# Performance work log

Measured on AMD Instinct MI355X. Metric: run time of the kernel, lower is better.

## Reference

```python
import jax, jax.numpy as jnp
import numpy as np

B, L, D = 16, 4096, 512


def setup_inputs() -> dict:
    key = jax.random.key(0)
    ks = jax.random.split(key, 8)
    s = 1.0 / np.sqrt(D)
    x = jax.random.normal(ks[0], (B, L, D), dtype=jnp.float32)
    Wk = jax.random.normal(ks[1], (D, D), dtype=jnp.float32) * s
    Wq = jax.random.normal(ks[2], (D, D), dtype=jnp.float32) * s
    Wv = jax.random.normal(ks[3], (D, D), dtype=jnp.float32) * s
    bk = jnp.zeros((D,), jnp.float32)
    bq = jnp.zeros((D,), jnp.float32)
    bv = jnp.zeros((D,), jnp.float32)
    lens = jax.random.randint(ks[4], (B,), 1, L + 1, dtype=jnp.int32)
    return {"x": x, "Wk": Wk, "bk": bk, "Wq": Wq, "bq": bq,
            "Wv": Wv, "bv": bv, "lens": lens}


def reference(x, Wk, bk, Wq, bq, Wv, bv, lens):
    # Dropout is identity in eval mode.
    x_k = jnp.tanh(jnp.einsum('bld,ed->ble', x, Wk) + bk)  # [B,L,D]
    x_q = jnp.tanh(jnp.einsum('bld,ed->ble', x, Wq) + bq)
    x_v = jnp.tanh(jnp.einsum('bld,ed->ble', x, Wv) + bv)
    # sum_j (x_k_i . x_q_j) == x_k_i . sum_j x_q_j  (algebraic collapse of the L x L bmm)
    q_sum = x_q.sum(axis=1)                                # [B,D]
    w = jnp.einsum('bld,bd->bl', x_k, q_sum) / (D ** 0.5)  # [B,L]
    pad = jnp.arange(L)[None, :] >= lens[:, None]          # True at padding
    w = jnp.where(pad, -jnp.inf, w)
    w = jax.nn.softmax(w, axis=1)                          # [B,L]
    # (x_v * w[...,None]).sum(-1) == x_v.sum(-1) * w
    return x_v.sum(axis=-1) * w                            # [B,L]
```

## Files before the change

kernel.cpp:

```cpp
#include <hip/hip_runtime.h>
#include <hip/hip_bf16.h>

typedef __attribute__((ext_vector_type(4)))  int   i32x4;
typedef __attribute__((ext_vector_type(16))) int   i32x16;
typedef __attribute__((ext_vector_type(16))) float f32x16;
typedef __attribute__((ext_vector_type(8)))  short short8;

#define SC1 (1.0f/4096.0f)
#define SC2 (1.0f/524288.0f)

static __device__ __forceinline__ float ftanh(float x) {
  float e = __builtin_amdgcn_exp2f(x * 2.885390081777927f);
  return 1.0f - 2.0f * __builtin_amdgcn_rcpf(e + 1.0f);
}
static __device__ __forceinline__ unsigned short bf16_rn(float f) {
  unsigned u = __float_as_uint(f);
  u += 0x7FFFu + ((u >> 16) & 1u);
  return (unsigned short)(u >> 16);
}
static __device__ __forceinline__ void quant2(float x, float sc, float inv, float losc,
                                              int& hi, int& lo) {
  float t  = __builtin_fmaf(x, sc, 12582912.0f);
  hi = __float_as_int(t) - 0x4B400000;
  float hf = t - 12582912.0f;
  float r  = __builtin_fmaf(hf, -inv, x);
  float t2 = __builtin_fmaf(r, losc, 12582912.0f);
  lo = __float_as_int(t2) - 0x4B400000;
}
static __device__ __forceinline__ void gll16(const void* g, void* l) {
  __builtin_amdgcn_global_load_lds((const __attribute__((address_space(1))) unsigned int*)g,
                                   (__attribute__((address_space(3))) unsigned int*)l, 16, 0, 0);
}
#define MFMA_I8(ACC, A, B) \
  asm("v_mfma_i32_32x32x32_i8 %0, %1, %2, %0" : "+v"(ACC) : "v"(A), "v"(B))

__global__ void prep_w(const float* __restrict__ Wq, const float* __restrict__ Wk,
                       const float* __restrict__ Wv,
                       char* __restrict__ B1, char* __restrict__ B2) {
  int gid = blockIdx.x * 256 + threadIdx.x;
  if (gid < 65536) {
    int chunk = gid >> 12, g = gid & 4095;
    char* dst = B1 + chunk * 65536 + g * 16;
    if (g < 2048) {
      int sel = g >> 10;
      int gg = g & 1023, nt = gg >> 6, lane = gg & 63;
      const float* src = Wq + (size_t)(nt * 32 + (lane & 31)) * 512 + chunk * 32 + (lane >> 5) * 16;
      union { char b[16]; i32x4 v; } ob;
#pragma unroll
      for (int j = 0; j < 16; ++j) {
        int h, l; quant2(src[j], 256.f, 1.f / 256.f, 32768.f, h, l);
        ob.b[j] = (char)(sel ? l : h);
      }
      *(i32x4*)dst = ob.v;
    } else {
      int gg = g - 2048, nt = gg >> 7, ks = (gg >> 6) & 1, lane = gg & 63;
      const float* src = Wv + (size_t)(nt * 32 + (lane & 31)) * 512 + chunk * 32 + ks * 16 + (lane >> 5) * 8;
      union { unsigned short s[8]; i32x4 v; } ob;
#pragma unroll
      for (int j = 0; j < 8; ++j) ob.s[j] = bf16_rn(src[j]);
      *(i32x4*)dst = ob.v;
    }
  } else {
    int gid2 = gid - 65536;
    int chunk = gid2 >> 11, g = gid2 & 2047;
    char* dst = B2 + chunk * 32768 + g * 16;
    int sel = g >> 10, gg = g & 1023, nt = gg >> 6, lane = gg & 63;
    const float* src = Wk + (size_t)(nt * 32 + (lane & 31)) * 512 + chunk * 32 + (lane >> 5) * 16;
    union { char b[16]; i32x4 v; } ob;
#pragma unroll
    for (int j = 0; j < 16; ++j) {
      int h, l; quant2(src[j], 256.f, 1.f / 256.f, 32768.f, h, l);
      ob.b[j] = (char)(sel ? l : h);
    }
    *(i32x4*)dst = ob.v;
  }
}

static __device__ __forceinline__ void stageAi8(char* Ab, int tid, float4 xv) {
  const int row = tid >> 3, d0 = (tid & 7) * 4;
  const int mt = row >> 5, l31 = row & 31;
  int h0, l0, h1, l1, h2, l2, h3, l3;
  quant2(xv.x, 16.f, 0.0625f, 2048.f, h0, l0);
  quant2(xv.y, 16.f, 0.0625f, 2048.f, h1, l1);
  quant2(xv.z, 16.f, 0.0625f, 2048.f, h2, l2);
  quant2(xv.w, 16.f, 0.0625f, 2048.f, h3, l3);
  unsigned wh = (h0 & 255) | ((h1 & 255) << 8) | ((h2 & 255) << 16) | ((unsigned)(h3 & 255) << 24);
  unsigned wl = (l0 & 255) | ((l1 & 255) << 8) | ((l2 & 255) << 16) | ((unsigned)(l3 & 255) << 24);
  const int lane8 = (d0 >> 4) * 32 + l31, j = d0 & 15;
  *(unsigned*)(Ab + (mt * 64 + lane8) * 16 + j) = wh;
  *(unsigned*)(Ab + 2048 + (mt * 64 + lane8) * 16 + j) = wl;
}

static __device__ __forceinline__ void stageAv(char* Ab, int tid, float4 xv) {
  const int row = tid >> 3, d0 = (tid & 7) * 4;
  const int mt = row >> 5, l31 = row & 31;
  unsigned long long b0 = bf16_rn(xv.x), b1 = bf16_rn(xv.y), b2 = bf16_rn(xv.z), b3 = bf16_rn(xv.w);
  unsigned long long vv = b0 | (b1 << 16) | (b2 << 32) | (b3 << 48);
  const int ks = d0 >> 4, rem = d0 & 15, hs8 = rem >> 3, j8 = rem & 7;
  *(unsigned long long*)(Ab + ((mt * 2 + ks) * 64 + hs8 * 32 + l31) * 16 + j8 * 2) = vv;
}

__global__ __launch_bounds__(512, 2) void pass_q(
    const float* __restrict__ x, const char* __restrict__ B1,
    const float* __restrict__ bq, float* __restrict__ qpart) {
  extern __shared__ char smem[];
  char* Bb0 = smem;            char* Bb1 = smem + 32768;
  char* Ab0 = smem + 65536;    char* Ab1 = smem + 69632;

  const int tid = threadIdx.x, lane = tid & 63, w = tid >> 6;
  const int l31 = lane & 31;
  const float* xrow = x + ((size_t)blockIdx.x * 64 + (tid >> 3)) * 512 + (tid & 7) * 4;

  i32x16 q1[2][2] = {}; i32x16 q2[2][2] = {};

  float4 xcur = *(const float4*)(xrow);
  stageAi8(Ab0, tid, xcur);
  {
    const char* src = B1 + tid * 16;
    char* dst = Bb0 + tid * 16;
#pragma unroll
    for (int i = 0; i < 4; ++i) gll16(src + i * 8192, dst + i * 8192);
  }
  xcur = *(const float4*)(xrow + 32);

#pragma unroll 1
  for (int c = 0; c < 16; ++c) {
    const int p = c & 1;
    char* Bc = p ? Bb1 : Bb0;  char* Bn = p ? Bb0 : Bb1;
    char* Ac = p ? Ab1 : Ab0;  char* An = p ? Ab0 : Ab1;
    __syncthreads();
    if (c < 15) {
      const char* src = B1 + (size_t)(c + 1) * 65536 + tid * 16;
      char* dst = Bn + tid * 16;
#pragma unroll
      for (int i = 0; i < 4; ++i) gll16(src + i * 8192, dst + i * 8192);
    }
    float4 xnext = xcur;
    if (c < 14) xnext = *(const float4*)(xrow + (c + 2) * 32);
    if (c < 15) stageAi8(An, tid, xcur);

    const int lo16 = lane * 16;
    i32x4 aqh0 = *(const i32x4*)(Ac + lo16);
    i32x4 aqh1 = *(const i32x4*)(Ac + 1024 + lo16);
    i32x4 aql0 = *(const i32x4*)(Ac + 2048 + lo16);
    i32x4 aql1 = *(const i32x4*)(Ac + 3072 + lo16);
    __builtin_amdgcn_s_setprio(1);
#pragma unroll
    for (int nn = 0; nn < 2; ++nn) {
      const int nt = w * 2 + nn;
      i32x4 bh = *(const i32x4*)(Bc + nt * 1024 + lo16);
      i32x4 bl = *(const i32x4*)(Bc + 16384 + nt * 1024 + lo16);
      MFMA_I8(q1[0][nn], aqh0, bh);
      MFMA_I8(q2[0][nn], aqh0, bl);
      MFMA_I8(q2[0][nn], aql0, bh);
      MFMA_I8(q1[1][nn], aqh1, bh);
      MFMA_I8(q2[1][nn], aqh1, bl);
      MFMA_I8(q2[1][nn], aql1, bh);
    }
    __builtin_amdgcn_s_setprio(0);
    xcur = xnext;
  }

#pragma unroll
  for (int nn = 0; nn < 2; ++nn) {
    const int col = (w * 2 + nn) * 32 + l31;
    const float bc = bq[col];
    float cs = 0.f;
#pragma unroll
    for (int mt = 0; mt < 2; ++mt)
#pragma unroll
      for (int r = 0; r < 16; ++r)
        cs += ftanh(__builtin_fmaf((float)q1[mt][nn][r], SC1,
                    __builtin_fmaf((float)q2[mt][nn][r], SC2, bc)));
    cs += __shfl_xor(cs, 32);
    if (lane < 32) qpart[(size_t)blockIdx.x * 512 + col] = cs;
  }
}

__global__ __launch_bounds__(512, 2) void pass_v(
    const float* __restrict__ x, const char* __restrict__ B1,
    const float* __restrict__ bv, float* __restrict__ svout) {
  extern __shared__ char smem[];
  char* Bb0 = smem;            char* Bb1 = smem + 32768;
  char* Ab0 = smem + 65536;    char* Ab1 = smem + 69632;
  float* redv = (float*)(smem + 73728);

  const int tid = threadIdx.x, lane = tid & 63, w = tid >> 6;
  const int l31 = lane & 31, hs = lane >> 5;
  const float* xrow = x + ((size_t)blockIdx.x * 64 + (tid >> 3)) * 512 + (tid & 7) * 4;

  f32x16 accv[2][2] = {};

  float4 xcur = *(const float4*)(xrow);
  stageAv(Ab0, tid, xcur);
  {
    const char* src = B1 + 32768 + tid * 16;
    char* dst = Bb0 + tid * 16;
#pragma unroll
    for (int i = 0; i < 4; ++i) gll16(src + i * 8192, dst + i * 8192);
  }
  xcur = *(const float4*)(xrow + 32);

#pragma unroll 1
  for (int c = 0; c < 16; ++c) {
    const int p = c & 1;
    char* Bc = p ? Bb1 : Bb0;  char* Bn = p ? Bb0 : Bb1;
    char* Ac = p ? Ab1 : Ab0;  char* An = p ? Ab0 : Ab1;
    __syncthreads();
    if (c < 15) {
      const char* src = B1 + (size_t)(c + 1) * 65536 + 32768 + tid * 16;
      char* dst = Bn + tid * 16;
#pragma unroll
      for (int i = 0; i < 4; ++i) gll16(src + i * 8192, dst + i * 8192);
    }
    float4 xnext = xcur;
    if (c < 14) xnext = *(const float4*)(xrow + (c + 2) * 32);
    if (c < 15) stageAv(An, tid, xcur);

    const int lo16 = lane * 16;
    __builtin_amdgcn_s_setprio(1);
#pragma unroll
    for (int ks = 0; ks < 2; ++ks) {
      short8 av0 = *(const short8*)(Ac + (0 * 2 + ks) * 1024 + lo16);
      short8 av1 = *(const short8*)(Ac + (1 * 2 + ks) * 1024 + lo16);
#pragma unroll
      for (int nn = 0; nn < 2; ++nn) {
        const int nt = w * 2 + nn;
        short8 bvf = *(const short8*)(Bc + (nt * 2 + ks) * 1024 + lo16);
        accv[0][nn] = __builtin_amdgcn_mfma_f32_32x32x16_bf16(av0, bvf, accv[0][nn], 0, 0, 0);
        accv[1][nn] = __builtin_amdgcn_mfma_f32_32x32x16_bf16(av1, bvf, accv[1][nn], 0, 0, 0);
      }
    }
    __builtin_amdgcn_s_setprio(0);
    xcur = xnext;
  }

  const float bv0 = bv[(w * 2 + 0) * 32 + l31];
  const float bv1 = bv[(w * 2 + 1) * 32 + l31];
  __syncthreads();
#pragma unroll
  for (int mt = 0; mt < 2; ++mt)
#pragma unroll
    for (int r = 0; r < 16; ++r) {
      float s = ftanh(accv[mt][0][r] + bv0) + ftanh(accv[mt][1][r] + bv1);
#pragma unroll
      for (int off = 1; off <= 16; off <<= 1) s += __shfl_xor(s, off);
      if (l31 == 0) redv[w * 64 + mt * 32 + (r & 3) + 8 * (r >> 2) + 4 * hs] = s;
    }
  __syncthreads();
  if (tid < 64) {
    float s = 0.f;
#pragma unroll
    for (int j = 0; j < 8; ++j) s += redv[j * 64 + tid];
    svout[(size_t)blockIdx.x * 64 + tid] = s;
  }
}

__global__ __launch_bounds__(512, 2) void pass_k(
    const float* __restrict__ x, const char* __restrict__ B2,
    const float* __restrict__ bk, const float* __restrict__ q_sum,
    float* __restrict__ scores) {
  extern __shared__ char smem[];
  char* Bb0 = smem;           char* Bb1 = smem + 32768;
  char* Ab0 = smem + 65536;   char* Ab1 = smem + 69632;
  float* redk = (float*)(smem + 73728);

  const int tid = threadIdx.x, lane = tid & 63, w = tid >> 6;
  const int l31 = lane & 31, hs = lane >> 5;
  const float* xrow = x + ((size_t)blockIdx.x * 64 + (tid >> 3)) * 512 + (tid & 7) * 4;

  i32x16 k1[2][2] = {}; i32x16 k2[2][2] = {};

  float4 xcur = *(const float4*)(xrow);
  stageAi8(Ab0, tid, xcur);
  {
    const char* src = B2 + tid * 16;
    char* dst = Bb0 + tid * 16;
#pragma unroll
    for (int i = 0; i < 4; ++i) gll16(src + i * 8192, dst + i * 8192);
  }
  xcur = *(const float4*)(xrow + 32);

#pragma unroll 1
  for (int c = 0; c < 16; ++c) {
    const int p = c & 1;
    char* Bc = p ? Bb1 : Bb0;  char* Bn = p ? Bb0 : Bb1;
    char* Ac = p ? Ab1 : Ab0;  char* An = p ? Ab0 : Ab1;
    __syncthreads();
    if (c < 15) {
      const char* src = B2 + (size_t)(c + 1) * 32768 + tid * 16;
      char* dst = Bn + tid * 16;
#pragma unroll
      for (int i = 0; i < 4; ++i) gll16(src + i * 8192, dst + i * 8192);
    }
    float4 xnext = xcur;
    if (c < 14) xnext = *(const float4*)(xrow + (c + 2) * 32);
    if (c < 15) stageAi8(An, tid, xcur);

    const int lo16 = lane * 16;
    i32x4 ah0 = *(const i32x4*)(Ac + lo16);
    i32x4 ah1 = *(const i32x4*)(Ac + 1024 + lo16);
    i32x4 al0 = *(const i32x4*)(Ac + 2048 + lo16);
    i32x4 al1 = *(const i32x4*)(Ac + 3072 + lo16);
    __builtin_amdgcn_s_setprio(1);
#pragma unroll
    for (int nn = 0; nn < 2; ++nn) {
      const int nt = w * 2 + nn;
      i32x4 bh = *(const i32x4*)(Bc + nt * 1024 + lo16);
      i32x4 bl = *(const i32x4*)(Bc + 16384 + nt * 1024 + lo16);
      MFMA_I8(k1[0][nn], ah0, bh);
      MFMA_I8(k2[0][nn], ah0, bl);
      MFMA_I8(k2[0][nn], al0, bh);
      MFMA_I8(k1[1][nn], ah1, bh);
      MFMA_I8(k2[1][nn], ah1, bl);
      MFMA_I8(k2[1][nn], al1, bh);
    }
    __builtin_amdgcn_s_setprio(0);
    xcur = xnext;
  }

  const int b = blockIdx.x >> 6;
  const int c0 = (w * 2 + 0) * 32 + l31, c1 = (w * 2 + 1) * 32 + l31;
  const float qs0 = q_sum[b * 512 + c0], qs1 = q_sum[b * 512 + c1];
  const float bk0 = bk[c0], bk1 = bk[c1];
  __syncthreads();
#pragma unroll
  for (int mt = 0; mt < 2; ++mt)
#pragma unroll
    for (int r = 0; r < 16; ++r) {
      float p0 = __builtin_fmaf((float)k1[mt][0][r], SC1,
                 __builtin_fmaf((float)k2[mt][0][r], SC2, bk0));
      float p1 = __builtin_fmaf((float)k1[mt][1][r], SC1,
                 __builtin_fmaf((float)k2[mt][1][r], SC2, bk1));
      float s = ftanh(p0) * qs0 + ftanh(p1) * qs1;
#pragma unroll
      for (int off = 1; off <= 16; off <<= 1) s += __shfl_xor(s, off);
      if (l31 == 0) redk[w * 64 + mt * 32 + (r & 3) + 8 * (r >> 2) + 4 * hs] = s;
    }
  __syncthreads();
  if (tid < 64) {
    float s = 0.f;
#pragma unroll
    for (int j = 0; j < 8; ++j) s += redk[j * 64 + tid];
    scores[(size_t)blockIdx.x * 64 + tid] = s;
  }
}

__global__ void reduce_q(const float* __restrict__ qpart, float* __restrict__ q_sum) {
  int b = blockIdx.x, e = threadIdx.x;
  const float* p = qpart + (size_t)b * 64 * 512 + e;
  float s = 0.f;
#pragma unroll 4
  for (int j = 0; j < 64; ++j) s += p[j * 512];
  q_sum[b * 512 + e] = s;
}

__global__ void softmax_out(const float* __restrict__ scores,
                            const float* __restrict__ sv,
                            const int* __restrict__ lens,
                            float* __restrict__ out) {
  const int b = blockIdx.x, tid = threadIdx.x;
  const int lane = tid & 63, wid = tid >> 6;
  const int len = lens[b];
  const float scale = 0.04419417382415922f;
  __shared__ float sb[4], sb2[4];

  float sreg[16];
  const float* sc = scores + (size_t)b * 4096;
#pragma unroll
  for (int j = 0; j < 16; ++j) sreg[j] = sc[tid + j * 256] * scale;

  float m = -1e30f;
#pragma unroll
  for (int j = 0; j < 16; ++j)
    if (tid + j * 256 < len) m = fmaxf(m, sreg[j]);
#pragma unroll
  for (int off = 32; off >= 1; off >>= 1) m = fmaxf(m, __shfl_xor(m, off));
  if (lane == 0) sb[wid] = m;
  __syncthreads();
  m = fmaxf(fmaxf(sb[0], sb[1]), fmaxf(sb[2], sb[3]));

  float s = 0.f;
#pragma unroll
  for (int j = 0; j < 16; ++j)
    if (tid + j * 256 < len) s += expf(sreg[j] - m);
#pragma unroll
  for (int off = 32; off >= 1; off >>= 1) s += __shfl_xor(s, off);
  if (lane == 0) sb2[wid] = s;
  __syncthreads();
  const float inv = 1.f / (sb2[0] + sb2[1] + sb2[2] + sb2[3]);

  const float* svb = sv + (size_t)b * 4096;
  float* ob = out + (size_t)b * 4096;
#pragma unroll
  for (int j = 0; j < 16; ++j) {
    int l = tid + j * 256;
    ob[l] = (l < len) ? svb[l] * expf(sreg[j] - m) * inv : 0.0f;
  }
}

extern "C" void kernel_launch(void* const* d_in, const int* in_sizes, int n_in,
                              void* d_out, int out_size, void* d_ws, size_t ws_size,
                              hipStream_t stream) {
  const float* x  = (const float*)d_in[0];
  const float* Wk = (const float*)d_in[1];
  const float* bk = (const float*)d_in[2];
  const float* Wq = (const float*)d_in[3];
  const float* bq = (const float*)d_in[4];
  const float* Wv = (const float*)d_in[5];
  const float* bv = (const float*)d_in[6];
  const int* lens = (const int*)d_in[7];
  float* out = (float*)d_out;

  char* ws = (char*)d_ws;
  char*  B1     = ws;
  char*  B2     = ws + 1048576;
  float* qpart  = (float*)(ws + 1572864);
  float* q_sum  = (float*)(ws + 3670016);
  float* svbuf  = (float*)(ws + 3702784);
  float* scores = (float*)(ws + 3964928);

  prep_w<<<384, 256, 0, stream>>>(Wq, Wk, Wv, B1, B2);
  pass_q<<<1024, 512, 73728, stream>>>(x, B1, bq, qpart);
  pass_v<<<1024, 512, 75776, stream>>>(x, B1, bv, svbuf);
  reduce_q<<<16, 512, 0, stream>>>(qpart, q_sum);
  pass_k<<<1024, 512, 75776, stream>>>(x, B2, bk, q_sum, scores);
  softmax_out<<<16, 256, 0, stream>>>(scores, svbuf, lens, out);
}
```

Baseline: 246.3 us.

## Split the projection passes into four column-group blocks with smaller LDS footprint

Each of pass_q, pass_v and pass_k now launches 4096 blocks of 256 threads, and each block computes a 128-column slice of the output instead of all 512 columns. This shrinks LDS per block and lets more blocks fit per CU, aiming for better latency hiding. The V and K passes now write per-column-group partial sums, which softmax_out adds together. The cost is that every x tile is read and quantized four times per pass, which relies on cache reuse to avoid extra HBM traffic. The s_setprio hints are also removed.

Result: slower. 300.6 us (+22.0%).

```diff
diff --git a/kernel.cpp b/kernel.cpp
--- a/kernel.cpp
+++ b/kernel.cpp
@@ -76,8 +76,7 @@
   }
 }
 
-static __device__ __forceinline__ void stageAi8(char* Ab, int tid, float4 xv) {
-  const int row = tid >> 3, d0 = (tid & 7) * 4;
+static __device__ __forceinline__ void stA8(char* Ab, int row, int d0, float4 xv) {
   const int mt = row >> 5, l31 = row & 31;
   int h0, l0, h1, l1, h2, l2, h3, l3;
   quant2(xv.x, 16.f, 0.0625f, 2048.f, h0, l0);
@@ -90,9 +89,7 @@
   *(unsigned*)(Ab + (mt * 64 + lane8) * 16 + j) = wh;
   *(unsigned*)(Ab + 2048 + (mt * 64 + lane8) * 16 + j) = wl;
 }
-
-static __device__ __forceinline__ void stageAv(char* Ab, int tid, float4 xv) {
-  const int row = tid >> 3, d0 = (tid & 7) * 4;
+static __device__ __forceinline__ void stAv(char* Ab, int row, int d0, float4 xv) {
   const int mt = row >> 5, l31 = row & 31;
   unsigned long long b0 = bf16_rn(xv.x), b1 = bf16_rn(xv.y), b2 = bf16_rn(xv.z), b3 = bf16_rn(xv.w);
   unsigned long long vv = b0 | (b1 << 16) | (b2 << 32) | (b3 << 48);
@@ -100,28 +97,31 @@
   *(unsigned long long*)(Ab + ((mt * 2 + ks) * 64 + hs8 * 32 + l31) * 16 + j8 * 2) = vv;
 }
 
-__global__ __launch_bounds__(512, 2) void pass_q(
+__global__ __launch_bounds__(256, 3) void pass_q(
     const float* __restrict__ x, const char* __restrict__ B1,
     const float* __restrict__ bq, float* __restrict__ qpart) {
   extern __shared__ char smem[];
-  char* Bb0 = smem;            char* Bb1 = smem + 32768;
-  char* Ab0 = smem + 65536;    char* Ab1 = smem + 69632;
+  char* Bb0 = smem;           char* Bb1 = smem + 8192;
+  char* Ab0 = smem + 16384;   char* Ab1 = smem + 20480;
 
   const int tid = threadIdx.x, lane = tid & 63, w = tid >> 6;
   const int l31 = lane & 31;
-  const float* xrow = x + ((size_t)blockIdx.x * 64 + (tid >> 3)) * 512 + (tid & 7) * 4;
-
-  i32x16 q1[2][2] = {}; i32x16 q2[2][2] = {};
-
-  float4 xcur = *(const float4*)(xrow);
-  stageAi8(Ab0, tid, xcur);
+  const int tile = blockIdx.x & 1023, cg = blockIdx.x >> 10;
+  const int row = tid >> 2, d0 = (tid & 3) * 8;
+  const float* gxr = x + ((size_t)tile * 64 + row) * 512 + d0;
+
+  i32x16 q1[2] = {}, q2[2] = {};
+
+  float4 xa = *(const float4*)(gxr);
+  float4 xb = *(const float4*)(gxr + 4);
+  stA8(Ab0, row, d0, xa); stA8(Ab0, row, d0 + 4, xb);
   {
-    const char* src = B1 + tid * 16;
-    char* dst = Bb0 + tid * 16;
-#pragma unroll
-    for (int i = 0; i < 4; ++i) gll16(src + i * 8192, dst + i * 8192);
-  }
-  xcur = *(const float4*)(xrow + 32);
+    const char* src = B1 + cg * 4096 + tid * 16;
+    gll16(src, Bb0 + tid * 16);
+    gll16(src + 16384, Bb0 + 4096 + tid * 16);
+  }
+  xa = *(const float4*)(gxr + 32);
+  xb = *(const float4*)(gxr + 36);
 
 #pragma unroll 1
   for (int c = 0; c < 16; ++c) {
@@ -130,76 +130,72 @@
     char* Ac = p ? Ab1 : Ab0;  char* An = p ? Ab0 : Ab1;
     __syncthreads();
     if (c < 15) {
-      const char* src = B1 + (size_t)(c + 1) * 65536 + tid * 16;
-      char* dst = Bn + tid * 16;
-#pragma unroll
-      for (int i = 0; i < 4; ++i) gll16(src + i * 8192, dst + i * 8192);
-    }
-    float4 xnext = xcur;
-    if (c < 14) xnext = *(const float4*)(xrow + (c + 2) * 32);
-    if (c < 15) stageAi8(An, tid, xcur);
+      const char* src = B1 + (size_t)(c + 1) * 65536 + cg * 4096 + tid * 16;
+      gll16(src, Bn + tid * 16);
+      gll16(src + 16384, Bn + 4096 + tid * 16);
+    }
+    float4 xna = xa, xnb = xb;
+    if (c < 14) {
+      xna = *(const float4*)(gxr + (c + 2) * 32);
+      xnb = *(const float4*)(gxr + (c + 2) * 32 + 4);
+    }
+    if (c < 15) { stA8(An, row, d0, xa); stA8(An, row, d0 + 4, xb); }
 
     const int lo16 = lane * 16;
-    i32x4 aqh0 = *(const i32x4*)(Ac + lo16);
-    i32x4 aqh1 = *(const i32x4*)(Ac + 1024 + lo16);
-    i32x4 aql0 = *(const i32x4*)(Ac + 2048 + lo16);
-    i32x4 aql1 = *(const i32x4*)(Ac + 3072 + lo16);
-    __builtin_amdgcn_s_setprio(1);
-#pragma unroll
-    for (int nn = 0; nn < 2; ++nn) {
-      const int nt = w * 2 + nn;
-      i32x4 bh = *(const i32x4*)(Bc + nt * 1024 + lo16);
-      i32x4 bl = *(const i32x4*)(Bc + 16384 + nt * 1024 + lo16);
-      MFMA_I8(q1[0][nn], aqh0, bh);
-      MFMA_I8(q2[0][nn], aqh0, bl);
-      MFMA_I8(q2[0][nn], aql0, bh);
-      MFMA_I8(q1[1][nn], aqh1, bh);
-      MFMA_I8(q2[1][nn], aqh1, bl);
-      MFMA_I8(q2[1][nn], aql1, bh);
-    }
-    __builtin_amdgcn_s_setprio(0);
-    xcur = xnext;
-  }
-
-#pragma unroll
-  for (int nn = 0; nn < 2; ++nn) {
-    const int col = (w * 2 + nn) * 32 + l31;
-    const float bc = bq[col];
-    float cs = 0.f;
-#pragma unroll
-    for (int mt = 0; mt < 2; ++mt)
-#pragma unroll
-      for (int r = 0; r < 16; ++r)
-        cs += ftanh(__builtin_fmaf((float)q1[mt][nn][r], SC1,
-                    __builtin_fmaf((float)q2[mt][nn][r], SC2, bc)));
-    cs += __shfl_xor(cs, 32);
-    if (lane < 32) qpart[(size_t)blockIdx.x * 512 + col] = cs;
-  }
-}
-
-__global__ __launch_bounds__(512, 2) void pass_v(
+    i32x4 ah0 = *(const i32x4*)(Ac + lo16);
+    i32x4 ah1 = *(const i32x4*)(Ac + 1024 + lo16);
+    i32x4 al0 = *(const i32x4*)(Ac + 2048 + lo16);
+    i32x4 al1 = *(const i32x4*)(Ac + 3072 + lo16);
+    i32x4 bh = *(const i32x4*)(Bc + w * 1024 + lo16);
+    i32x4 bl = *(const i32x4*)(Bc + 4096 + w * 1024 + lo16);
+    MFMA_I8(q1[0], ah0, bh);
+    MFMA_I8(q2[0], ah0, bl);
+    MFMA_I8(q2[0], al0, bh);
+    MFMA_I8(q1[1], ah1, bh);
+    MFMA_I8(q2[1], ah1, bl);
+    MFMA_I8(q2[1], al1, bh);
+    xa = xna; xb = xnb;
+  }
+
+  const int col = cg * 128 + w * 32 + l31;
+  const float bc = bq[col];
+  float cs = 0.f;
+#pragma unroll
+  for (int mt = 0; mt < 2; ++mt)
+#pragma unroll
+    for (int r = 0; r < 16; ++r)
+      cs += ftanh(__builtin_fmaf((float)q1[mt][r], SC1,
+                  __builtin_fmaf((float)q2[mt][r], SC2, bc)));
+  cs += __shfl_xor(cs, 32);
+  if (lane < 32) qpart[(size_t)tile * 512 + col] = cs;
+}
+
+__global__ __launch_bounds__(256, 4) void pass_v(
     const float* __restrict__ x, const char* __restrict__ B1,
-    const float* __restrict__ bv, float* __restrict__ svout) {
+    const float* __restrict__ bv, float* __restrict__ vpart) {
   extern __shared__ char smem[];
-  char* Bb0 = smem;            char* Bb1 = smem + 32768;
-  char* Ab0 = smem + 65536;    char* Ab1 = smem + 69632;
-  float* redv = (float*)(smem + 73728);
+  char* Bb0 = smem;           char* Bb1 = smem + 8192;
+  char* Ab0 = smem + 16384;   char* Ab1 = smem + 20480;
+  float* redv = (float*)(smem + 24576);
 
   const int tid = threadIdx.x, lane = tid & 63, w = tid >> 6;
   const int l31 = lane & 31, hs = lane >> 5;
-  const float* xrow = x + ((size_t)blockIdx.x * 64 + (tid >> 3)) * 512 + (tid & 7) * 4;
-
-  f32x16 accv[2][2] = {};
-
-  float4 xcur = *(const float4*)(xrow);
-  stageAv(Ab0, tid, xcur);
+  const int tile = blockIdx.x & 1023, cg = blockIdx.x >> 10;
+  const int row = tid >> 2, d0 = (tid & 3) * 8;
+  const float* gxr = x + ((size_t)tile * 64 + row) * 512 + d0;
+
+  f32x16 accv[2] = {};
+
+  float4 xa = *(const float4*)(gxr);
+  float4 xb = *(const float4*)(gxr + 4);
+  stAv(Ab0, row, d0, xa); stAv(Ab0, row, d0 + 4, xb);
   {
-    const char* src = B1 + 32768 + tid * 16;
-    char* dst = Bb0 + tid * 16;
-#pragma unroll
-    for (int i = 0; i < 4; ++i) gll16(src + i * 8192, dst + i * 8192);
-  }
-  xcur = *(const float4*)(xrow + 32);
+    const char* src = B1 + 32768 + cg * 8192 + tid * 16;
+    gll16(src, Bb0 + tid * 16);
+    gll16(src + 4096, Bb0 + 4096 + tid * 16);
+  }
+  xa = *(const float4*)(gxr + 32);
+  xb = *(const float4*)(gxr + 36);
 
 #pragma unroll 1
   for (int c = 0; c < 16; ++c) {
@@ -208,78 +204,74 @@
     char* Ac = p ? Ab1 : Ab0;  char* An = p ? Ab0 : Ab1;
     __syncthreads();
     if (c < 15) {
-      const char* src = B1 + (size_t)(c + 1) * 65536 + 32768 + tid * 16;
-      char* dst = Bn + tid * 16;
-#pragma unroll
-      for (int i = 0; i < 4; ++i) gll16(src + i * 8192, dst + i * 8192);
-    }
-    float4 xnext = xcur;
-    if (c < 14) xnext = *(const float4*)(xrow + (c + 2) * 32);
-    if (c < 15) stageAv(An, tid, xcur);
+      const char* src = B1 + (size_t)(c + 1) * 65536 + 32768 + cg * 8192 + tid * 16;
+      gll16(src, Bn + tid * 16);
+      gll16(src + 4096, Bn + 4096 + tid * 16);
+    }
+    float4 xna = xa, xnb = xb;
+    if (c < 14) {
+      xna = *(const float4*)(gxr + (c + 2) * 32);
+      xnb = *(const float4*)(gxr + (c + 2) * 32 + 4);
+    }
+    if (c < 15) { stAv(An, row, d0, xa); stAv(An, row, d0 + 4, xb); }
 
     const int lo16 = lane * 16;
-    __builtin_amdgcn_s_setprio(1);
 #pragma unroll
     for (int ks = 0; ks < 2; ++ks) {
       short8 av0 = *(const short8*)(Ac + (0 * 2 + ks) * 1024 + lo16);
       short8 av1 = *(const short8*)(Ac + (1 * 2 + ks) * 1024 + lo16);
-#pragma unroll
-      for (int nn = 0; nn < 2; ++nn) {
-        const int nt = w * 2 + nn;
-        short8 bvf = *(const short8*)(Bc + (nt * 2 + ks) * 1024 + lo16);
-        accv[0][nn] = __builtin_amdgcn_mfma_f32_32x32x16_bf16(av0, bvf, accv[0][nn], 0, 0, 0);
-        accv[1][nn] = __builtin_amdgcn_mfma_f32_32x32x16_bf16(av1, bvf, accv[1][nn], 0, 0, 0);
-      }
-    }
-    __builtin_amdgcn_s_setprio(0);
-    xcur = xnext;
-  }
-
-  const float bv0 = bv[(w * 2 + 0) * 32 + l31];
-  const float bv1 = bv[(w * 2 + 1) * 32 + l31];
+      short8 bvf = *(const short8*)(Bc + (w * 2 + ks) * 1024 + lo16);
+      accv[0] = __builtin_amdgcn_mfma_f32_32x32x16_bf16(av0, bvf, accv[0], 0, 0, 0);
+      accv[1] = __builtin_amdgcn_mfma_f32_32x32x16_bf16(av1, bvf, accv[1], 0, 0, 0);
+    }
+    xa = xna; xb = xnb;
+  }
+
+  const float bvc = bv[cg * 128 + w * 32 + l31];
   __syncthreads();
 #pragma unroll
   for (int mt = 0; mt < 2; ++mt)
 #pragma unroll
     for (int r = 0; r < 16; ++r) {
-      float s = ftanh(accv[mt][0][r] + bv0) + ftanh(accv[mt][1][r] + bv1);
+      float s = ftanh(accv[mt][r] + bvc);
 #pragma unroll
       for (int off = 1; off <= 16; off <<= 1) s += __shfl_xor(s, off);
       if (l31 == 0) redv[w * 64 + mt * 32 + (r & 3) + 8 * (r >> 2) + 4 * hs] = s;
     }
   __syncthreads();
   if (tid < 64) {
-    float s = 0.f;
-#pragma unroll
-    for (int j = 0; j < 8; ++j) s += redv[j * 64 + tid];
-    svout[(size_t)blockIdx.x * 64 + tid] = s;
-  }
-}
-
-__global__ __launch_bounds__(512, 2) void pass_k(
+    float s = redv[tid] + redv[64 + tid] + redv[128 + tid] + redv[192 + tid];
+    vpart[(size_t)cg * 65536 + (size_t)tile * 64 + tid] = s;
+  }
+}
+
+__global__ __launch_bounds__(256, 3) void pass_k(
     const float* __restrict__ x, const char* __restrict__ B2,
     const float* __restrict__ bk, const float* __restrict__ q_sum,
-    float* __restrict__ scores) {
+    float* __restrict__ spart) {
   extern __shared__ char smem[];
-  char* Bb0 = smem;           char* Bb1 = smem + 32768;
-  char* Ab0 = smem + 65536;   char* Ab1 = smem + 69632;
-  float* redk = (float*)(smem + 73728);
+  char* Bb0 = smem;           char* Bb1 = smem + 8192;
+  char* Ab0 = smem + 16384;   char* Ab1 = smem + 20480;
+  float* redk = (float*)(smem + 24576);
 
   const int tid = threadIdx.x, lane = tid & 63, w = tid >> 6;
   const int l31 = lane & 31, hs = lane >> 5;
-  const float* xrow = x + ((size_t)blockIdx.x * 64 + (tid >> 3)) * 512 + (tid & 7) * 4;
-
-  i32x16 k1[2][2] = {}; i32x16 k2[2][2] = {};
-
-  float4 xcur = *(const float4*)(xrow);
-  stageAi8(Ab0, tid, xcur);
+  const int tile = blockIdx.x & 1023, cg = blockIdx.x >> 10;
+  const int row = tid >> 2, d0 = (tid & 3) * 8;
+  const float* gxr = x + ((size_t)tile * 64 + row) * 512 + d0;
+
+  i32x16 k1[2] = {}, k2[2] = {};
+
+  float4 xa = *(const float4*)(gxr);
+  float4 xb = *(const float4*)(gxr + 4);
+  stA8(Ab0, row, d0, xa); stA8(Ab0, row, d0 + 4, xb);
   {
-    const char* src = B2 + tid * 16;
-    char* dst = Bb0 + tid * 16;
-#pragma unroll
-    for (int i = 0; i < 4; ++i) gll16(src + i * 8192, dst + i * 8192);
-  }
-  xcur = *(const float4*)(xrow + 32);
+    const char* src = B2 + cg * 4096 + tid * 16;
+    gll16(src, Bb0 + tid * 16);
+    gll16(src + 16384, Bb0 + 4096 + tid * 16);
+  }
+  xa = *(const float4*)(gxr + 32);
+  xb = *(const float4*)(gxr + 36);
 
 #pragma unroll 1
   for (int c = 0; c < 16; ++c) {
@@ -288,61 +280,53 @@
     char* Ac = p ? Ab1 : Ab0;  char* An = p ? Ab0 : Ab1;
     __syncthreads();
     if (c < 15) {
-      const char* src = B2 + (size_t)(c + 1) * 32768 + tid * 16;
-      char* dst = Bn + tid * 16;
-#pragma unroll
-      for (int i = 0; i < 4; ++i) gll16(src + i * 8192, dst + i * 8192);
-    }
-    float4 xnext = xcur;
-    if (c < 14) xnext = *(const float4*)(xrow + (c + 2) * 32);
-    if (c < 15) stageAi8(An, tid, xcur);
+      const char* src = B2 + (size_t)(c + 1) * 32768 + cg * 4096 + tid * 16;
+      gll16(src, Bn + tid * 16);
+      gll16(src + 16384, Bn + 4096 + tid * 16);
+    }
+    float4 xna = xa, xnb = xb;
+    if (c < 14) {
+      xna = *(const float4*)(gxr + (c + 2) * 32);
+      xnb = *(const float4*)(gxr + (c + 2) * 32 + 4);
+    }
+    if (c < 15) { stA8(An, row, d0, xa); stA8(An, row, d0 + 4, xb); }
 
     const int lo16 = lane * 16;
     i32x4 ah0 = *(const i32x4*)(Ac + lo16);
     i32x4 ah1 = *(const i32x4*)(Ac + 1024 + lo16);
     i32x4 al0 = *(const i32x4*)(Ac + 2048 + lo16);
     i32x4 al1 = *(const i32x4*)(Ac + 3072 + lo16);
-    __builtin_amdgcn_s_setprio(1);
-#pragma unroll
-    for (int nn = 0; nn < 2; ++nn) {
-      const int nt = w * 2 + nn;
-      i32x4 bh = *(const i32x4*)(Bc + nt * 1024 + lo16);
-      i32x4 bl = *(const i32x4*)(Bc + 16384 + nt * 1024 + lo16);
-      MFMA_I8(k1[0][nn], ah0, bh);
-      MFMA_I8(k2[0][nn], ah0, bl);
-      MFMA_I8(k2[0][nn], al0, bh);
-      MFMA_I8(k1[1][nn], ah1, bh);
-      MFMA_I8(k2[1][nn], ah1, bl);
-      MFMA_I8(k2[1][nn], al1, bh);
-    }
-    __builtin_amdgcn_s_setprio(0);
-    xcur = xnext;
-  }
-
-  const int b = blockIdx.x >> 6;
-  const int c0 = (w * 2 + 0) * 32 + l31, c1 = (w * 2 + 1) * 32 + l31;
-  const float qs0 = q_sum[b * 512 + c0], qs1 = q_sum[b * 512 + c1];
-  const float bk0 = bk[c0], bk1 = bk[c1];
+    i32x4 bh = *(const i32x4*)(Bc + w * 1024 + lo16);
+    i32x4 bl = *(const i32x4*)(Bc + 4096 + w * 1024 + lo16);
+    MFMA_I8(k1[0], ah0, bh);
+    MFMA_I8(k2[0], ah0, bl);
+    MFMA_I8(k2[0], al0, bh);
+    MFMA_I8(k1[1], ah1, bh);
+    MFMA_I8(k2[1], ah1, bl);
+    MFMA_I8(k2[1], al1, bh);
+    xa = xna; xb = xnb;
+  }
+
+  const int b = tile >> 6;
+  const int col = cg * 128 + w * 32 + l31;
+  const float qs = q_sum[b * 512 + col];
+  const float bkc = bk[col];
   __syncthreads();
 #pragma unroll
   for (int mt = 0; mt < 2; ++mt)
 #pragma unroll
     for (int r = 0; r < 16; ++r) {
-      float p0 = __builtin_fmaf((float)k1[mt][0][r], SC1,
-                 __builtin_fmaf((float)k2[mt][0][r], SC2, bk0));
-      float p1 = __builtin_fmaf((float)k1[mt][1][r], SC1,
-                 __builtin_fmaf((float)k2[mt][1][r], SC2, bk1));
-      float s = ftanh(p0) * qs0 + ftanh(p1) * qs1;
+      float pre = __builtin_fmaf((float)k1[mt][r], SC1,
+                  __builtin_fmaf((float)k2[mt][r], SC2, bkc));
+      float s = ftanh(pre) * qs;
 #pragma unroll
       for (int off = 1; off <= 16; off <<= 1) s += __shfl_xor(s, off);
       if (l31 == 0) redk[w * 64 + mt * 32 + (r & 3) + 8 * (r >> 2) + 4 * hs] = s;
     }
   __syncthreads();
   if (tid < 64) {
-    float s = 0.f;
-#pragma unroll
-    for (int j = 0; j < 8; ++j) s += redk[j * 64 + tid];
-    scores[(size_t)blockIdx.x * 64 + tid] = s;
+    float s = redk[tid] + redk[64 + tid] + redk[128 + tid] + redk[192 + tid];
+    spart[(size_t)cg * 65536 + (size_t)tile * 64 + tid] = s;
   }
 }
 
@@ -355,8 +339,8 @@
   q_sum[b * 512 + e] = s;
 }
 
-__global__ void softmax_out(const float* __restrict__ scores,
-                            const float* __restrict__ sv,
+__global__ void softmax_out(const float* __restrict__ spart,
+                            const float* __restrict__ vpart,
                             const int* __restrict__ lens,
                             float* __restrict__ out) {
   const int b = blockIdx.x, tid = threadIdx.x;
@@ -365,10 +349,13 @@
   const float scale = 0.04419417382415922f;
   __shared__ float sb[4], sb2[4];
 
-  float sreg[16];
-  const float* sc = scores + (size_t)b * 4096;
-#pragma unroll
-  for (int j = 0; j < 16; ++j) sreg[j] = sc[tid + j * 256] * scale;
+  float sreg[16], svreg[16];
+#pragma unroll
+  for (int j = 0; j < 16; ++j) {
+    size_t l = (size_t)b * 4096 + tid + j * 256;
+    sreg[j] = (spart[l] + spart[65536 + l] + spart[131072 + l] + spart[196608 + l]) * scale;
+    svreg[j] = vpart[l] + vpart[65536 + l] + vpart[131072 + l] + vpart[196608 + l];
+  }
 
   float m = -1e30f;
 #pragma unroll
@@ -390,12 +377,11 @@
   __syncthreads();
   const float inv = 1.f / (sb2[0] + sb2[1] + sb2[2] + sb2[3]);
 
-  const float* svb = sv + (size_t)b * 4096;
   float* ob = out + (size_t)b * 4096;
 #pragma unroll
   for (int j = 0; j < 16; ++j) {
     int l = tid + j * 256;
-    ob[l] = (l < len) ? svb[l] * expf(sreg[j] - m) * inv : 0.0f;
+    ob[l] = (l < len) ? svreg[j] * expf(sreg[j] - m) * inv : 0.0f;
   }
 }
 
@@ -417,13 +403,13 @@
   char*  B2     = ws + 1048576;
   float* qpart  = (float*)(ws + 1572864);
   float* q_sum  = (float*)(ws + 3670016);
-  float* svbuf  = (float*)(ws + 3702784);
-  float* scores = (float*)(ws + 3964928);
+  float* vpart  = (float*)(ws + 3702784);
+  float* spart  = (float*)(ws + 4751360);
 
   prep_w<<<384, 256, 0, stream>>>(Wq, Wk, Wv, B1, B2);
-  pass_q<<<1024, 512, 73728, stream>>>(x, B1, bq, qpart);
-  pass_v<<<1024, 512, 75776, stream>>>(x, B1, bv, svbuf);
+  pass_q<<<4096, 256, 24576, stream>>>(x, B1, bq, qpart);
+  pass_v<<<4096, 256, 25600, stream>>>(x, B1, bv, vpart);
   reduce_q<<<16, 512, 0, stream>>>(qpart, q_sum);
-  pass_k<<<1024, 512, 75776, stream>>>(x, B2, bk, q_sum, scores);
-  softmax_out<<<16, 256, 0, stream>>>(scores, svbuf, lens, out);
-}
+  pass_k<<<4096, 256, 25600, stream>>>(x, B2, bk, q_sum, spart);
+  softmax_out<<<16, 256, 0, stream>>>(spart, vpart, lens, out);
+}
```

## Halve row tile to 32 per block and double grid size

Applied to the files above, without the earlier changes.

Each of the three projection passes now handles 32 rows of x per block instead of 64, giving 2048 blocks, and only half the threads stage A. The full 512-column weight slab is still streamed into LDS per block, so total weight traffic through L2/LDS doubles relative to x rows. Launch bounds ask for 4 blocks per CU and setprio hints are removed, and reduce_q sums 128 partials. This trades weight reuse per block for more blocks and fewer accumulator registers per thread, but LDS use per block (~69KB) still limits residency.

Result: slower. 263.5 us (+7.0%).

```diff
diff --git a/kernel.cpp b/kernel.cpp
--- a/kernel.cpp
+++ b/kernel.cpp
@@ -76,9 +76,7 @@
   }
 }
 
-static __device__ __forceinline__ void stageAi8(char* Ab, int tid, float4 xv) {
-  const int row = tid >> 3, d0 = (tid & 7) * 4;
-  const int mt = row >> 5, l31 = row & 31;
+static __device__ __forceinline__ void stA8_32(char* Ab, int row, int d0, float4 xv) {
   int h0, l0, h1, l1, h2, l2, h3, l3;
   quant2(xv.x, 16.f, 0.0625f, 2048.f, h0, l0);
   quant2(xv.y, 16.f, 0.0625f, 2048.f, h1, l1);
@@ -86,42 +84,41 @@
   quant2(xv.w, 16.f, 0.0625f, 2048.f, h3, l3);
   unsigned wh = (h0 & 255) | ((h1 & 255) << 8) | ((h2 & 255) << 16) | ((unsigned)(h3 & 255) << 24);
   unsigned wl = (l0 & 255) | ((l1 & 255) << 8) | ((l2 & 255) << 16) | ((unsigned)(l3 & 255) << 24);
-  const int lane8 = (d0 >> 4) * 32 + l31, j = d0 & 15;
-  *(unsigned*)(Ab + (mt * 64 + lane8) * 16 + j) = wh;
-  *(unsigned*)(Ab + 2048 + (mt * 64 + lane8) * 16 + j) = wl;
-}
-
-static __device__ __forceinline__ void stageAv(char* Ab, int tid, float4 xv) {
-  const int row = tid >> 3, d0 = (tid & 7) * 4;
-  const int mt = row >> 5, l31 = row & 31;
+  const int lane8 = (d0 >> 4) * 32 + row, j = d0 & 15;
+  *(unsigned*)(Ab + lane8 * 16 + j) = wh;
+  *(unsigned*)(Ab + 1024 + lane8 * 16 + j) = wl;
+}
+static __device__ __forceinline__ void stAv_32(char* Ab, int row, int d0, float4 xv) {
   unsigned long long b0 = bf16_rn(xv.x), b1 = bf16_rn(xv.y), b2 = bf16_rn(xv.z), b3 = bf16_rn(xv.w);
   unsigned long long vv = b0 | (b1 << 16) | (b2 << 32) | (b3 << 48);
   const int ks = d0 >> 4, rem = d0 & 15, hs8 = rem >> 3, j8 = rem & 7;
-  *(unsigned long long*)(Ab + ((mt * 2 + ks) * 64 + hs8 * 32 + l31) * 16 + j8 * 2) = vv;
-}
-
-__global__ __launch_bounds__(512, 2) void pass_q(
+  *(unsigned long long*)(Ab + (ks * 64 + hs8 * 32 + row) * 16 + j8 * 2) = vv;
+}
+
+__global__ __launch_bounds__(512, 4) void pass_q(
     const float* __restrict__ x, const char* __restrict__ B1,
     const float* __restrict__ bq, float* __restrict__ qpart) {
   extern __shared__ char smem[];
-  char* Bb0 = smem;            char* Bb1 = smem + 32768;
-  char* Ab0 = smem + 65536;    char* Ab1 = smem + 69632;
+  char* Bb0 = smem;          char* Bb1 = smem + 32768;
+  char* Ab0 = smem + 65536;  char* Ab1 = smem + 67584;
 
   const int tid = threadIdx.x, lane = tid & 63, w = tid >> 6;
   const int l31 = lane & 31;
-  const float* xrow = x + ((size_t)blockIdx.x * 64 + (tid >> 3)) * 512 + (tid & 7) * 4;
-
-  i32x16 q1[2][2] = {}; i32x16 q2[2][2] = {};
-
-  float4 xcur = *(const float4*)(xrow);
-  stageAi8(Ab0, tid, xcur);
+  const int tile = blockIdx.x;
+  const int row = tid >> 3, d0 = (tid & 7) * 4;
+  const float* gxr = x + ((size_t)tile * 32 + row) * 512 + d0;
+
+  i32x16 q1[2] = {}, q2[2] = {};
+  float4 xcur = {};
+
+  if (tid < 256) { xcur = *(const float4*)(gxr); stA8_32(Ab0, row, d0, xcur); }
   {
     const char* src = B1 + tid * 16;
     char* dst = Bb0 + tid * 16;
 #pragma unroll
     for (int i = 0; i < 4; ++i) gll16(src + i * 8192, dst + i * 8192);
   }
-  xcur = *(const float4*)(xrow + 32);
+  if (tid < 256) xcur = *(const float4*)(gxr + 32);
 
 #pragma unroll 1
   for (int c = 0; c < 16; ++c) {
@@ -136,28 +133,23 @@
       for (int i = 0; i < 4; ++i) gll16(src + i * 8192, dst + i * 8192);
     }
     float4 xnext = xcur;
-    if (c < 14) xnext = *(const float4*)(xrow + (c + 2) * 32);
-    if (c < 15) stageAi8(An, tid, xcur);
+    if (tid < 256) {
+      if (c < 14) xnext = *(const float4*)(gxr + (c + 2) * 32);
+      if (c < 15) stA8_32(An, row, d0, xcur);
+    }
 
     const int lo16 = lane * 16;
-    i32x4 aqh0 = *(const i32x4*)(Ac + lo16);
-    i32x4 aqh1 = *(const i32x4*)(Ac + 1024 + lo16);
-    i32x4 aql0 = *(const i32x4*)(Ac + 2048 + lo16);
-    i32x4 aql1 = *(const i32x4*)(Ac + 3072 + lo16);
-    __builtin_amdgcn_s_setprio(1);
+    i32x4 ah = *(const i32x4*)(Ac + lo16);
+    i32x4 al = *(const i32x4*)(Ac + 1024 + lo16);
 #pragma unroll
     for (int nn = 0; nn < 2; ++nn) {
       const int nt = w * 2 + nn;
       i32x4 bh = *(const i32x4*)(Bc + nt * 1024 + lo16);
       i32x4 bl = *(const i32x4*)(Bc + 16384 + nt * 1024 + lo16);
-      MFMA_I8(q1[0][nn], aqh0, bh);
-      MFMA_I8(q2[0][nn], aqh0, bl);
-      MFMA_I8(q2[0][nn], aql0, bh);
-      MFMA_I8(q1[1][nn], aqh1, bh);
-      MFMA_I8(q2[1][nn], aqh1, bl);
-      MFMA_I8(q2[1][nn], aql1, bh);
-    }
-    __builtin_amdgcn_s_setprio(0);
+      MFMA_I8(q1[nn], ah, bh);
+      MFMA_I8(q2[nn], ah, bl);
+      MFMA_I8(q2[nn], al, bh);
+    }
     xcur = xnext;
   }
 
@@ -167,39 +159,39 @@
     const float bc = bq[col];
     float cs = 0.f;
 #pragma unroll
-    for (int mt = 0; mt < 2; ++mt)
-#pragma unroll
-      for (int r = 0; r < 16; ++r)
-        cs += ftanh(__builtin_fmaf((float)q1[mt][nn][r], SC1,
-                    __builtin_fmaf((float)q2[mt][nn][r], SC2, bc)));
+    for (int r = 0; r < 16; ++r)
+      cs += ftanh(__builtin_fmaf((float)q1[nn][r], SC1,
+                  __builtin_fmaf((float)q2[nn][r], SC2, bc)));
     cs += __shfl_xor(cs, 32);
-    if (lane < 32) qpart[(size_t)blockIdx.x * 512 + col] = cs;
-  }
-}
-
-__global__ __launch_bounds__(512, 2) void pass_v(
+    if (lane < 32) qpart[(size_t)tile * 512 + col] = cs;
+  }
+}
+
+__global__ __launch_bounds__(512, 4) void pass_v(
     const float* __restrict__ x, const char* __restrict__ B1,
     const float* __restrict__ bv, float* __restrict__ svout) {
   extern __shared__ char smem[];
-  char* Bb0 = smem;            char* Bb1 = smem + 32768;
-  char* Ab0 = smem + 65536;    char* Ab1 = smem + 69632;
-  float* redv = (float*)(smem + 73728);
+  char* Bb0 = smem;          char* Bb1 = smem + 32768;
+  char* Ab0 = smem + 65536;  char* Ab1 = smem + 67584;
+  float* redv = (float*)(smem + 69632);
 
   const int tid = threadIdx.x, lane = tid & 63, w = tid >> 6;
   const int l31 = lane & 31, hs = lane >> 5;
-  const float* xrow = x + ((size_t)blockIdx.x * 64 + (tid >> 3)) * 512 + (tid & 7) * 4;
-
-  f32x16 accv[2][2] = {};
-
-  float4 xcur = *(const float4*)(xrow);
-  stageAv(Ab0, tid, xcur);
+  const int tile = blockIdx.x;
+  const int row = tid >> 3, d0 = (tid & 7) * 4;
+  const float* gxr = x + ((size_t)tile * 32 + row) * 512 + d0;
+
+  f32x16 accv[2] = {};
+  float4 xcur = {};
+
+  if (tid < 256) { xcur = *(const float4*)(gxr); stAv_32(Ab0, row, d0, xcur); }
   {
     const char* src = B1 + 32768 + tid * 16;
     char* dst = Bb0 + tid * 16;
 #pragma unroll
     for (int i = 0; i < 4; ++i) gll16(src + i * 8192, dst + i * 8192);
   }
-  xcur = *(const float4*)(xrow + 32);
+  if (tid < 256) xcur = *(const float4*)(gxr + 32);
 
 #pragma unroll 1
   for (int c = 0; c < 16; ++c) {
@@ -214,24 +206,22 @@
       for (int i = 0; i < 4; ++i) gll16(src + i * 8192, dst + i * 8192);
     }
     float4 xnext = xcur;
-    if (c < 14) xnext = *(const float4*)(xrow + (c + 2) * 32);
-    if (c < 15) stageAv(An, tid, xcur);
+    if (tid < 256) {
+      if (c < 14) xnext = *(const float4*)(gxr + (c + 2) * 32);
+      if (c < 15) stAv_32(An, row, d0, xcur);
+    }
 
     const int lo16 = lane * 16;
-    __builtin_amdgcn_s_setprio(1);
 #pragma unroll
     for (int ks = 0; ks < 2; ++ks) {
-      short8 av0 = *(const short8*)(Ac + (0 * 2 + ks) * 1024 + lo16);
-      short8 av1 = *(const short8*)(Ac + (1 * 2 + ks) * 1024 + lo16);
+      short8 av = *(const short8*)(Ac + ks * 1024 + lo16);
 #pragma unroll
       for (int nn = 0; nn < 2; ++nn) {
         const int nt = w * 2 + nn;
         short8 bvf = *(const short8*)(Bc + (nt * 2 + ks) * 1024 + lo16);
-        accv[0][nn] = __builtin_amdgcn_mfma_f32_32x32x16_bf16(av0, bvf, accv[0][nn], 0, 0, 0);
-        accv[1][nn] = __builtin_amdgcn_mfma_f32_32x32x16_bf16(av1, bvf, accv[1][nn], 0, 0, 0);
+        accv[nn] = __builtin_amdgcn_mfma_f32_32x32x16_bf16(av, bvf, accv[nn], 0, 0, 0);
       }
     }
-    __builtin_amdgcn_s_setprio(0);
     xcur = xnext;
   }
 
@@ -239,47 +229,47 @@
   const float bv1 = bv[(w * 2 + 1) * 32 + l31];
   __syncthreads();
 #pragma unroll
-  for (int mt = 0; mt < 2; ++mt)
-#pragma unroll
-    for (int r = 0; r < 16; ++r) {
-      float s = ftanh(accv[mt][0][r] + bv0) + ftanh(accv[mt][1][r] + bv1);
-#pragma unroll
-      for (int off = 1; off <= 16; off <<= 1) s += __shfl_xor(s, off);
-      if (l31 == 0) redv[w * 64 + mt * 32 + (r & 3) + 8 * (r >> 2) + 4 * hs] = s;
-    }
-  __syncthreads();
-  if (tid < 64) {
+  for (int r = 0; r < 16; ++r) {
+    float s = ftanh(accv[0][r] + bv0) + ftanh(accv[1][r] + bv1);
+#pragma unroll
+    for (int off = 1; off <= 16; off <<= 1) s += __shfl_xor(s, off);
+    if (l31 == 0) redv[w * 32 + (r & 3) + 8 * (r >> 2) + 4 * hs] = s;
+  }
+  __syncthreads();
+  if (tid < 32) {
     float s = 0.f;
 #pragma unroll
-    for (int j = 0; j < 8; ++j) s += redv[j * 64 + tid];
-    svout[(size_t)blockIdx.x * 64 + tid] = s;
-  }
-}
-
-__global__ __launch_bounds__(512, 2) void pass_k(
+    for (int j = 0; j < 8; ++j) s += redv[j * 32 + tid];
+    svout[(size_t)tile * 32 + tid] = s;
+  }
+}
+
+__global__ __launch_bounds__(512, 4) void pass_k(
     const float* __restrict__ x, const char* __restrict__ B2,
     const float* __restrict__ bk, const float* __restrict__ q_sum,
     float* __restrict__ scores) {
   extern __shared__ char smem[];
-  char* Bb0 = smem;           char* Bb1 = smem + 32768;
-  char* Ab0 = smem + 65536;   char* Ab1 = smem + 69632;
-  float* redk = (float*)(smem + 73728);
+  char* Bb0 = smem;          char* Bb1 = smem + 32768;
+  char* Ab0 = smem + 65536;  char* Ab1 = smem + 67584;
+  float* redk = (float*)(smem + 69632);
 
   const int tid = threadIdx.x, lane = tid & 63, w = tid >> 6;
   const int l31 = lane & 31, hs = lane >> 5;
-  const float* xrow = x + ((size_t)blockIdx.x * 64 + (tid >> 3)) * 512 + (tid & 7) * 4;
-
-  i32x16 k1[2][2] = {}; i32x16 k2[2][2] = {};
-
-  float4 xcur = *(const float4*)(xrow);
-  stageAi8(Ab0, tid, xcur);
+  const int tile = blockIdx.x;
+  const int row = tid >> 3, d0 = (tid & 7) * 4;
+  const float* gxr = x + ((size_t)tile * 32 + row) * 512 + d0;
+
+  i32x16 k1[2] = {}, k2[2] = {};
+  float4 xcur = {};
+
+  if (tid < 256) { xcur = *(const float4*)(gxr); stA8_32(Ab0, row, d0, xcur); }
   {
     const char* src = B2 + tid * 16;
     char* dst = Bb0 + tid * 16;
 #pragma unroll
     for (int i = 0; i < 4; ++i) gll16(src + i * 8192, dst + i * 8192);
   }
-  xcur = *(const float4*)(xrow + 32);
+  if (tid < 256) xcur = *(const float4*)(gxr + 32);
 
 #pragma unroll 1
   for (int c = 0; c < 16; ++c) {
@@ -294,64 +284,57 @@
       for (int i = 0; i < 4; ++i) gll16(src + i * 8192, dst + i * 8192);
     }
     float4 xnext = xcur;
-    if (c < 14) xnext = *(const float4*)(xrow + (c + 2) * 32);
-    if (c < 15) stageAi8(An, tid, xcur);
+    if (tid < 256) {
+      if (c < 14) xnext = *(const float4*)(gxr + (c + 2) * 32);
+      if (c < 15) stA8_32(An, row, d0, xcur);
+    }
 
     const int lo16 = lane * 16;
-    i32x4 ah0 = *(const i32x4*)(Ac + lo16);
-    i32x4 ah1 = *(const i32x4*)(Ac + 1024 + lo16);
-    i32x4 al0 = *(const i32x4*)(Ac + 2048 + lo16);
-    i32x4 al1 = *(const i32x4*)(Ac + 3072 + lo16);
-    __builtin_amdgcn_s_setprio(1);
+    i32x4 ah = *(const i32x4*)(Ac + lo16);
+    i32x4 al = *(const i32x4*)(Ac + 1024 + lo16);
 #pragma unroll
     for (int nn = 0; nn < 2; ++nn) {
       const int nt = w * 2 + nn;
       i32x4 bh = *(const i32x4*)(Bc + nt * 1024 + lo16);
       i32x4 bl = *(const i32x4*)(Bc + 16384 + nt * 1024 + lo16);
-      MFMA_I8(k1[0][nn], ah0, bh);
-      MFMA_I8(k2[0][nn], ah0, bl);
-      MFMA_I8(k2[0][nn], al0, bh);
-      MFMA_I8(k1[1][nn], ah1, bh);
-      MFMA_I8(k2[1][nn], ah1, bl);
-      MFMA_I8(k2[1][nn], al1, bh);
-    }
-    __builtin_amdgcn_s_setprio(0);
+      MFMA_I8(k1[nn], ah, bh);
+      MFMA_I8(k2[nn], ah, bl);
+      MFMA_I8(k2[nn], al, bh);
+    }
     xcur = xnext;
   }
 
-  const int b = blockIdx.x >> 6;
+  const int b = tile >> 7;
   const int c0 = (w * 2 + 0) * 32 + l31, c1 = (w * 2 + 1) * 32 + l31;
   const float qs0 = q_sum[b * 512 + c0], qs1 = q_sum[b * 512 + c1];
   const float bk0 = bk[c0], bk1 = bk[c1];
   __syncthreads();
 #pragma unroll
-  for (int mt = 0; mt < 2; ++mt)
-#pragma unroll
-    for (int r = 0; r < 16; ++r) {
-      float p0 = __builtin_fmaf((float)k1[mt][0][r], SC1,
-                 __builtin_fmaf((float)k2[mt][0][r], SC2, bk0));
-      float p1 = __builtin_fmaf((float)k1[mt][1][r], SC1,
-                 __builtin_fmaf((float)k2[mt][1][r], SC2, bk1));
-      float s = ftanh(p0) * qs0 + ftanh(p1) * qs1;
-#pragma unroll
-      for (int off = 1; off <= 16; off <<= 1) s += __shfl_xor(s, off);
-      if (l31 == 0) redk[w * 64 + mt * 32 + (r & 3) + 8 * (r >> 2) + 4 * hs] = s;
-    }
-  __syncthreads();
-  if (tid < 64) {
+  for (int r = 0; r < 16; ++r) {
+    float p0 = __builtin_fmaf((float)k1[0][r], SC1,
+               __builtin_fmaf((float)k2[0][r], SC2, bk0));
+    float p1 = __builtin_fmaf((float)k1[1][r], SC1,
+               __builtin_fmaf((float)k2[1][r], SC2, bk1));
+    float s = ftanh(p0) * qs0 + ftanh(p1) * qs1;
+#pragma unroll
+    for (int off = 1; off <= 16; off <<= 1) s += __shfl_xor(s, off);
+    if (l31 == 0) redk[w * 32 + (r & 3) + 8 * (r >> 2) + 4 * hs] = s;
+  }
+  __syncthreads();
+  if (tid < 32) {
     float s = 0.f;
 #pragma unroll
-    for (int j = 0; j < 8; ++j) s += redk[j * 64 + tid];
-    scores[(size_t)blockIdx.x * 64 + tid] = s;
+    for (int j = 0; j < 8; ++j) s += redk[j * 32 + tid];
+    scores[(size_t)tile * 32 + tid] = s;
   }
 }
 
 __global__ void reduce_q(const float* __restrict__ qpart, float* __restrict__ q_sum) {
   int b = blockIdx.x, e = threadIdx.x;
-  const float* p = qpart + (size_t)b * 64 * 512 + e;
+  const float* p = qpart + (size_t)b * 128 * 512 + e;
   float s = 0.f;
 #pragma unroll 4
-  for (int j = 0; j < 64; ++j) s += p[j * 512];
+  for (int j = 0; j < 128; ++j) s += p[j * 512];
   q_sum[b * 512 + e] = s;
 }
 
@@ -416,14 +399,14 @@
   char*  B1     = ws;
   char*  B2     = ws + 1048576;
   float* qpart  = (float*)(ws + 1572864);
-  float* q_sum  = (float*)(ws + 3670016);
-  float* svbuf  = (float*)(ws + 3702784);
-  float* scores = (float*)(ws + 3964928);
+  float* q_sum  = (float*)(ws + 5767168);
+  float* svbuf  = (float*)(ws + 5799936);
+  float* scores = (float*)(ws + 6062080);
 
   prep_w<<<384, 256, 0, stream>>>(Wq, Wk, Wv, B1, B2);
-  pass_q<<<1024, 512, 73728, stream>>>(x, B1, bq, qpart);
-  pass_v<<<1024, 512, 75776, stream>>>(x, B1, bv, svbuf);
+  pass_q<<<2048, 512, 69632, stream>>>(x, B1, bq, qpart);
+  pass_v<<<2048, 512, 70656, stream>>>(x, B1, bv, svbuf);
   reduce_q<<<16, 512, 0, stream>>>(qpart, q_sum);
-  pass_k<<<1024, 512, 75776, stream>>>(x, B2, bk, q_sum, scores);
+  pass_k<<<2048, 512, 70656, stream>>>(x, B2, bk, q_sum, scores);
   softmax_out<<<16, 256, 0, stream>>>(scores, svbuf, lens, out);
 }
```
